# Optimization experiments

Measured on AMD Instinct MI355X. Metric: run time of the kernel, lower is better.

Reference implementation:

```python
import jax, jax.numpy as jnp
import numpy as np


def setup_inputs() -> dict:
    key = jax.random.key(0)
    k1, k2, k3, k4 = jax.random.split(key, 4)
    T, B, D_in, D_out = 512, 128, 512, 512
    X = jax.random.normal(k1, (T, B, D_in), dtype=jnp.float32)
    # torch nn.Linear default init: U(-1/sqrt(fan_in), 1/sqrt(fan_in))
    lim_in = 1.0 / np.sqrt(D_in)
    lim_h = 1.0 / np.sqrt(D_out)
    W_in = jax.random.uniform(k2, (D_out, D_in), jnp.float32, -lim_in, lim_in)
    W_h = jax.random.uniform(k3, (D_out, D_out), jnp.float32, -lim_h, lim_h)
    b_h = jax.random.uniform(k4, (D_out,), jnp.float32, -lim_h, lim_h)
    return {"X": X, "W_in": W_in, "W_h": W_h, "b_h": b_h}


def reference(X, W_in, W_h, b_h):
    # X: [T, B, D_in]. h_{t+1} = sigmoid(x_t @ W_in^T + h_t @ W_h^T + b_h)
    B = X.shape[1]
    D_out = W_h.shape[0]
    # Precompute all input projections in one big GEMM (same math).
    Xproj = jnp.einsum('tbi,oi->tbo', X, W_in)  # [T, B, D_out]
    h0 = jnp.zeros((B, D_out), dtype=X.dtype)

    def step(h, xp):
        h_new = jax.nn.sigmoid(xp + h @ W_h.T + b_h)
        return h_new, None

    h_last, _ = jax.lax.scan(step, h0, Xproj)
    return h_last
```

## Files before the change

### kernel.cpp

```cpp
#include <hip/hip_runtime.h>
#include <hip/hip_bf16.h>
#include <stdint.h>

typedef _Float16 f16;
typedef _Float16 f16x2 __attribute__((ext_vector_type(2)));
typedef _Float16 f16x4 __attribute__((ext_vector_type(4)));
typedef _Float16 f16x8 __attribute__((ext_vector_type(8)));
typedef float f32x4 __attribute__((ext_vector_type(4)));
typedef int   i32x4 __attribute__((ext_vector_type(4)));

#define T_STEPS 512
#define BATCH   128
#define DD      512
#define LOG2E   1.44269504088896f

#define XP_OFF  0
#define WF_OFF  (67108864)
#define WHQ_OFF (67108864 + 524288)
#define SC_OFF  (67108864 + 524288 + 262144)

__device__ __forceinline__ f16x2 pk(float a, float b) {
    return __builtin_bit_cast(f16x2, __builtin_amdgcn_cvt_pkrtz(a, b));
}

__device__ __forceinline__ float fast_exp2(float x) {
#if __has_builtin(__builtin_amdgcn_exp2f)
    return __builtin_amdgcn_exp2f(x);
#else
    return exp2f(x);
#endif
}

__device__ __forceinline__ float fast_rcp(float x) {
#if __has_builtin(__builtin_amdgcn_rcpf)
    return __builtin_amdgcn_rcpf(x);
#else
    return 1.0f / x;
#endif
}

__device__ __forceinline__ uint32_t pack_u8(float s, int pos, uint32_t old) {
#if __has_builtin(__builtin_amdgcn_cvt_pk_u8_f32)
    return __builtin_amdgcn_cvt_pk_u8_f32(s, pos, old);
#else
    return old | (((uint32_t)(int)s & 0xFF) << (8 * pos));
#endif
}

#define GLDS(g, l) __builtin_amdgcn_global_load_lds(                               \
        (const __attribute__((address_space(1))) void*)(g),                        \
        (__attribute__((address_space(3))) void*)(l), 16, 0, 0)

__global__ __launch_bounds__(256) void prep_kernel(
        const float* __restrict__ Win, f16* __restrict__ Wf) {
    int idx = blockIdx.x * 256 + threadIdx.x;
    if (idx < 262144) Wf[idx] = (f16)Win[idx];
}

__global__ __launch_bounds__(64) void quant_kernel(
        const float* __restrict__ Wh, char* __restrict__ Whq, float* __restrict__ scales) {
    const int o = blockIdx.x, t = threadIdx.x;
    const float* row = Wh + (size_t)o * 512;
    float v[8];
    float m = 0.f;
#pragma unroll
    for (int j = 0; j < 8; j++) { v[j] = row[t * 8 + j]; m = fmaxf(m, fabsf(v[j])); }
#pragma unroll
    for (int off = 32; off > 0; off >>= 1) m = fmaxf(m, __shfl_xor(m, off));
    if (t == 0) scales[o] = -LOG2E * m * (1.0f / (127.0f * 127.0f));
    const float inv = 127.0f / m;
    const int rt = o >> 4, rl = o & 15;
    const int k0 = t * 8;
    const int ks = k0 >> 6, qq = (k0 >> 4) & 3, j0 = k0 & 15;
    const int l = qq * 16 + rl;
    char* dst = Whq + ((size_t)((rt * 8 + ks) * 64 + l)) * 16 + j0;
#pragma unroll
    for (int j = 0; j < 8; j++) dst[j] = (char)rintf(v[j] * inv);
}

__global__ __launch_bounds__(512, 4) void gemm_kernel(
        const float* __restrict__ X, const f16* __restrict__ Wf,
        const float* __restrict__ bias, f16* __restrict__ Xp) {
    const int tid = threadIdx.x;
    const int l = tid & 63, w = tid >> 6;
    const int q = l >> 4, rl = l & 15;
    const int wm = w >> 2, wn = w & 3;
    const int blk = blockIdx.x;
    const int xcd = blk & 7, idx = blk >> 3;
    const int m_blk = (xcd * 64 + (idx >> 2)) * 128;
    const int n_blk = (idx & 3) * 128;

    __shared__ __align__(16) float As[2][128 * 32];
    __shared__ __align__(16) f16   Bs[2][128 * 32];

    const float* aSrc[2];
#pragma unroll
    for (int c = 0; c < 2; c++)
        aSrc[c] = X + (size_t)(m_blk + w * 16 + c * 8 + (l >> 3)) * 512
                    + (((l & 7) ^ (l >> 3)) << 2);
    const f16* bSrc = Wf + (size_t)(n_blk + w * 16 + (l >> 2)) * 512
                         + (((l & 3) ^ ((l >> 3) & 3)) << 3);

    f32x4 acc[4][2] = {};
    const int swA0 = (((2 * q)     ^ (rl & 7)) << 2);
    const int swA1 = (((2 * q + 1) ^ (rl & 7)) << 2);
    const int swB  = ((q ^ ((rl >> 1) & 3)) << 3);

#pragma unroll
    for (int c = 0; c < 2; c++) GLDS(aSrc[c], &As[0][(w * 16 + c * 8) * 32]);
    GLDS(bSrc, &Bs[0][(w * 16) * 32]);

    for (int t = 0; t < 16; ++t) {
        const int cur = t & 1;
        __syncthreads();
        if (t < 15) {
            const int kf = (t + 1) * 32;
#pragma unroll
            for (int c = 0; c < 2; c++) GLDS(aSrc[c] + kf, &As[cur ^ 1][(w * 16 + c * 8) * 32]);
            GLDS(bSrc + kf, &Bs[cur ^ 1][(w * 16) * 32]);
        }
        f16x8 af4[4], bf4[2];
#pragma unroll
        for (int i = 0; i < 4; i++) {
            const int row = wm * 64 + i * 16 + rl;
            const float4 h0 = *(const float4*)&As[cur][row * 32 + swA0];
            const float4 h1 = *(const float4*)&As[cur][row * 32 + swA1];
            f16x2 p0 = pk(h0.x, h0.y), p1 = pk(h0.z, h0.w);
            f16x2 p2 = pk(h1.x, h1.y), p3 = pk(h1.z, h1.w);
            f16x8 tv;
            tv[0] = p0[0]; tv[1] = p0[1]; tv[2] = p1[0]; tv[3] = p1[1];
            tv[4] = p2[0]; tv[5] = p2[1]; tv[6] = p3[0]; tv[7] = p3[1];
            af4[i] = tv;
        }
#pragma unroll
        for (int j = 0; j < 2; j++) {
            const int row = wn * 32 + j * 16 + rl;
            bf4[j] = *(const f16x8*)&Bs[cur][row * 32 + swB];
        }
#pragma unroll
        for (int i = 0; i < 4; i++)
#pragma unroll
            for (int j = 0; j < 2; j++)
                acc[i][j] = __builtin_amdgcn_mfma_f32_16x16x32_f16(bf4[j], af4[i], acc[i][j], 0, 0, 0);
    }
#pragma unroll
    for (int j = 0; j < 2; j++) {
        const float4 b4 = *(const float4*)&bias[n_blk + wn * 32 + j * 16 + q * 4];
        const float bb[4] = {b4.x, b4.y, b4.z, b4.w};
#pragma unroll
        for (int i = 0; i < 4; i++) {
            const int m = m_blk + wm * 64 + i * 16 + rl;
            f16x4 v;
#pragma unroll
            for (int r = 0; r < 4; r++)
                v[r] = (f16)(-LOG2E * (acc[i][j][r] + bb[r]));
            *(f16x4*)(Xp + (size_t)m * 512 + n_blk + wn * 32 + j * 16 + q * 4) = v;
        }
    }
}

__global__ __launch_bounds__(1024) void rnn_kernel(
        const char* __restrict__ Whq, const float* __restrict__ scales,
        const f16* __restrict__ Xp, float* __restrict__ out) {
    const int wg = blockIdx.x;
    const int tid = threadIdx.x;
    const int l = tid & 63, w = tid >> 6;
    const int bl = l & 15;
    const int q = l >> 4;
    const int b = wg * 16 + bl;

    __shared__ __align__(16) uint32_t hT[2][2048];

    i32x4 af[2][8];
    {
        const i32x4* wp = (const i32x4*)Whq;
#pragma unroll
        for (int mt = 0; mt < 2; mt++)
#pragma unroll
            for (int ks = 0; ks < 8; ks++)
                af[mt][ks] = wp[((w * 2 + mt) * 8 + ks) * 64 + l];
    }
    float sc[2][4];
#pragma unroll
    for (int mt = 0; mt < 2; mt++)
#pragma unroll
        for (int r = 0; r < 4; r++)
            sc[mt][r] = scales[w * 32 + mt * 16 + q * 4 + r];

    for (int i = tid; i < 2048; i += 1024) hT[0][i] = 0u;
    __syncthreads();

    const f16* xpb = Xp + (size_t)b * 512 + w * 32 + q * 4;
    f16x4 xn0 = *(const f16x4*)(xpb);
    f16x4 xn1 = *(const f16x4*)(xpb + 16);

    const float K127 = 1.0f / 127.0f;
    for (int t = 0; t < T_STEPS; t++) {
        f16x4 xc0 = xn0, xc1 = xn1;
        const size_t tn = (size_t)(t < T_STEPS - 1 ? t + 1 : t) * (BATCH * 512);
        xn0 = *(const f16x4*)(xpb + tn);
        xn1 = *(const f16x4*)(xpb + tn + 16);

        const int rb = t & 1;
        const uint32_t* hrow = &hT[rb][l * 4];
        uint32_t* hwr = &hT[1 - rb][w * 128 + bl * 4 + q];

        i32x4 bfr[8];
#pragma unroll
        for (int ks = 0; ks < 8; ks++)
            bfr[ks] = *(const i32x4*)(hrow + ks * 256);

        i32x4 acc0 = {}, acc1 = {};
        __builtin_amdgcn_s_setprio(1);
#pragma unroll
        for (int ks = 0; ks < 8; ks++)
            acc0 = __builtin_amdgcn_mfma_i32_16x16x64_i8(af[0][ks], bfr[ks], acc0, 0, 0, 0);

        uint32_t pk0 = 0;
#pragma unroll
        for (int r = 0; r < 4; r++) {
            float tt = fmaf((float)acc0[r], sc[0][r], (float)xc0[r]);
            float e  = fast_exp2(tt);
            float eq = fmaf(e, K127, K127);
            float sg = fast_rcp(eq) + 0.5f;
            pk0 = pack_u8(sg, r, pk0);
        }
        hwr[0] = pk0;

#pragma unroll
        for (int ks = 0; ks < 8; ks++)
            acc1 = __builtin_amdgcn_mfma_i32_16x16x64_i8(af[1][ks], bfr[ks], acc1, 0, 0, 0);
        __builtin_amdgcn_s_setprio(0);

        uint32_t pk1 = 0;
#pragma unroll
        for (int r = 0; r < 4; r++) {
            float tt = fmaf((float)acc1[r], sc[1][r], (float)xc1[r]);
            float e  = fast_exp2(tt);
            float eq = fmaf(e, K127, K127);
            float sg = fast_rcp(eq) + 0.5f;
            pk1 = pack_u8(sg, r, pk1);
        }
        hwr[64] = pk1;
        __syncthreads();
    }
#pragma unroll
    for (int mt = 0; mt < 2; mt++) {
        uint32_t pkq = hT[T_STEPS & 1][w * 128 + mt * 64 + bl * 4 + q];
        float4 o;
        o.x = (float)((pkq      ) & 0xFF) * K127;
        o.y = (float)((pkq >>  8) & 0xFF) * K127;
        o.z = (float)((pkq >> 16) & 0xFF) * K127;
        o.w = (float)((pkq >> 24) & 0xFF) * K127;
        *(float4*)(out + (size_t)b * 512 + w * 32 + mt * 16 + q * 4) = o;
    }
}

extern "C" void kernel_launch(void* const* d_in, const int* in_sizes, int n_in,
                              void* d_out, int out_size, void* d_ws, size_t ws_size,
                              hipStream_t stream) {
    const float* X   = (const float*)d_in[0];
    const float* Win = (const float*)d_in[1];
    const float* Wh  = (const float*)d_in[2];
    const float* bh  = (const float*)d_in[3];
    float* out = (float*)d_out;
    char* ws = (char*)d_ws;
    f16* Xp      = (f16*)(ws + XP_OFF);
    f16* Wf      = (f16*)(ws + WF_OFF);
    char* Whq    = (char*)(ws + WHQ_OFF);
    float* Sc    = (float*)(ws + SC_OFF);

    prep_kernel<<<1024, 256, 0, stream>>>(Win, Wf);
    quant_kernel<<<512, 64, 0, stream>>>(Wh, Whq, Sc);
    gemm_kernel<<<2048, 512, 0, stream>>>(X, Wf, bh, Xp);
    rnn_kernel<<<8, 1024, 0, stream>>>(Whq, Sc, Xp, out);
}
```

Measured before the change: 707.8 us.

## Halve RNN workgroup to 8 waves and retile input-projection GEMM to 64x128

The recurrent kernel now uses 8 waves per workgroup instead of 16. Each wave holds four 16-row output tiles of the int8 weight in registers and runs 32 MFMAs per step, which halves the number of waves meeting at each per-step barrier. The GEMM is retiled to 64x128 blocks with 256 threads and 4096 blocks, with each wave computing a 32x64 sub-tile. The intent is to cut per-timestep synchronisation cost in the serial recurrence, at the price of a longer MFMA chain per wave and doubled weight-register pressure.

```diff
diff --git a/kernel.cpp b/kernel.cpp
--- a/kernel.cpp
+++ b/kernel.cpp
@@ -78,19 +78,19 @@
     for (int j = 0; j < 8; j++) dst[j] = (char)rintf(v[j] * inv);
 }
 
-__global__ __launch_bounds__(512, 4) void gemm_kernel(
+__global__ __launch_bounds__(256, 4) void gemm_kernel(
         const float* __restrict__ X, const f16* __restrict__ Wf,
         const float* __restrict__ bias, f16* __restrict__ Xp) {
     const int tid = threadIdx.x;
     const int l = tid & 63, w = tid >> 6;
     const int q = l >> 4, rl = l & 15;
-    const int wm = w >> 2, wn = w & 3;
+    const int wm = w >> 1, wn = w & 1;
     const int blk = blockIdx.x;
     const int xcd = blk & 7, idx = blk >> 3;
-    const int m_blk = (xcd * 64 + (idx >> 2)) * 128;
+    const int m_blk = (xcd * 128 + (idx >> 2)) * 64;
     const int n_blk = (idx & 3) * 128;
 
-    __shared__ __align__(16) float As[2][128 * 32];
+    __shared__ __align__(16) float As[2][64 * 32];
     __shared__ __align__(16) f16   Bs[2][128 * 32];
 
     const float* aSrc[2];
@@ -98,17 +98,21 @@
     for (int c = 0; c < 2; c++)
         aSrc[c] = X + (size_t)(m_blk + w * 16 + c * 8 + (l >> 3)) * 512
                     + (((l & 7) ^ (l >> 3)) << 2);
-    const f16* bSrc = Wf + (size_t)(n_blk + w * 16 + (l >> 2)) * 512
-                         + (((l & 3) ^ ((l >> 3) & 3)) << 3);
-
-    f32x4 acc[4][2] = {};
+    const f16* bSrc[2];
+#pragma unroll
+    for (int c = 0; c < 2; c++)
+        bSrc[c] = Wf + (size_t)(n_blk + c * 64 + w * 16 + (l >> 2)) * 512
+                     + (((l & 3) ^ ((l >> 3) & 3)) << 3);
+
+    f32x4 acc[2][4] = {};
     const int swA0 = (((2 * q)     ^ (rl & 7)) << 2);
     const int swA1 = (((2 * q + 1) ^ (rl & 7)) << 2);
     const int swB  = ((q ^ ((rl >> 1) & 3)) << 3);
 
 #pragma unroll
     for (int c = 0; c < 2; c++) GLDS(aSrc[c], &As[0][(w * 16 + c * 8) * 32]);
-    GLDS(bSrc, &Bs[0][(w * 16) * 32]);
+#pragma unroll
+    for (int c = 0; c < 2; c++) GLDS(bSrc[c], &Bs[0][(c * 64 + w * 16) * 32]);
 
     for (int t = 0; t < 16; ++t) {
         const int cur = t & 1;
@@ -117,12 +121,13 @@
             const int kf = (t + 1) * 32;
 #pragma unroll
             for (int c = 0; c < 2; c++) GLDS(aSrc[c] + kf, &As[cur ^ 1][(w * 16 + c * 8) * 32]);
-            GLDS(bSrc + kf, &Bs[cur ^ 1][(w * 16) * 32]);
-        }
-        f16x8 af4[4], bf4[2];
-#pragma unroll
-        for (int i = 0; i < 4; i++) {
-            const int row = wm * 64 + i * 16 + rl;
+#pragma unroll
+            for (int c = 0; c < 2; c++) GLDS(bSrc[c] + kf, &Bs[cur ^ 1][(c * 64 + w * 16) * 32]);
+        }
+        f16x8 af4[2], bf4[4];
+#pragma unroll
+        for (int i = 0; i < 2; i++) {
+            const int row = wm * 32 + i * 16 + rl;
             const float4 h0 = *(const float4*)&As[cur][row * 32 + swA0];
             const float4 h1 = *(const float4*)&As[cur][row * 32 + swA1];
             f16x2 p0 = pk(h0.x, h0.y), p1 = pk(h0.z, h0.w);
@@ -133,33 +138,33 @@
             af4[i] = tv;
         }
 #pragma unroll
-        for (int j = 0; j < 2; j++) {
-            const int row = wn * 32 + j * 16 + rl;
+        for (int j = 0; j < 4; j++) {
+            const int row = wn * 64 + j * 16 + rl;
             bf4[j] = *(const f16x8*)&Bs[cur][row * 32 + swB];
         }
 #pragma unroll
-        for (int i = 0; i < 4; i++)
-#pragma unroll
-            for (int j = 0; j < 2; j++)
+        for (int i = 0; i < 2; i++)
+#pragma unroll
+            for (int j = 0; j < 4; j++)
                 acc[i][j] = __builtin_amdgcn_mfma_f32_16x16x32_f16(bf4[j], af4[i], acc[i][j], 0, 0, 0);
     }
 #pragma unroll
-    for (int j = 0; j < 2; j++) {
-        const float4 b4 = *(const float4*)&bias[n_blk + wn * 32 + j * 16 + q * 4];
+    for (int j = 0; j < 4; j++) {
+        const float4 b4 = *(const float4*)&bias[n_blk + wn * 64 + j * 16 + q * 4];
         const float bb[4] = {b4.x, b4.y, b4.z, b4.w};
 #pragma unroll
-        for (int i = 0; i < 4; i++) {
-            const int m = m_blk + wm * 64 + i * 16 + rl;
+        for (int i = 0; i < 2; i++) {
+            const int m = m_blk + wm * 32 + i * 16 + rl;
             f16x4 v;
 #pragma unroll
             for (int r = 0; r < 4; r++)
                 v[r] = (f16)(-LOG2E * (acc[i][j][r] + bb[r]));
-            *(f16x4*)(Xp + (size_t)m * 512 + n_blk + wn * 32 + j * 16 + q * 4) = v;
-        }
-    }
-}
-
-__global__ __launch_bounds__(1024) void rnn_kernel(
+            *(f16x4*)(Xp + (size_t)m * 512 + n_blk + wn * 64 + j * 16 + q * 4) = v;
+        }
+    }
+}
+
+__global__ __launch_bounds__(512, 2) void rnn_kernel(
         const char* __restrict__ Whq, const float* __restrict__ scales,
         const f16* __restrict__ Xp, float* __restrict__ out) {
     const int wg = blockIdx.x;
@@ -171,88 +176,78 @@
 
     __shared__ __align__(16) uint32_t hT[2][2048];
 
-    i32x4 af[2][8];
+    i32x4 af[4][8];
     {
         const i32x4* wp = (const i32x4*)Whq;
 #pragma unroll
-        for (int mt = 0; mt < 2; mt++)
+        for (int mt = 0; mt < 4; mt++)
 #pragma unroll
             for (int ks = 0; ks < 8; ks++)
-                af[mt][ks] = wp[((w * 2 + mt) * 8 + ks) * 64 + l];
-    }
-    float sc[2][4];
-#pragma unroll
-    for (int mt = 0; mt < 2; mt++)
+                af[mt][ks] = wp[((w * 4 + mt) * 8 + ks) * 64 + l];
+    }
+    float sc[4][4];
+#pragma unroll
+    for (int mt = 0; mt < 4; mt++)
 #pragma unroll
         for (int r = 0; r < 4; r++)
-            sc[mt][r] = scales[w * 32 + mt * 16 + q * 4 + r];
-
-    for (int i = tid; i < 2048; i += 1024) hT[0][i] = 0u;
+            sc[mt][r] = scales[w * 64 + mt * 16 + q * 4 + r];
+
+    for (int i = tid; i < 2048; i += 512) hT[0][i] = 0u;
     __syncthreads();
 
-    const f16* xpb = Xp + (size_t)b * 512 + w * 32 + q * 4;
-    f16x4 xn0 = *(const f16x4*)(xpb);
-    f16x4 xn1 = *(const f16x4*)(xpb + 16);
+    const f16* xpb = Xp + (size_t)b * 512 + w * 64 + q * 4;
+    f16x4 xn[4];
+#pragma unroll
+    for (int mt = 0; mt < 4; mt++) xn[mt] = *(const f16x4*)(xpb + mt * 16);
 
     const float K127 = 1.0f / 127.0f;
     for (int t = 0; t < T_STEPS; t++) {
-        f16x4 xc0 = xn0, xc1 = xn1;
+        f16x4 xc[4];
+#pragma unroll
+        for (int mt = 0; mt < 4; mt++) xc[mt] = xn[mt];
         const size_t tn = (size_t)(t < T_STEPS - 1 ? t + 1 : t) * (BATCH * 512);
-        xn0 = *(const f16x4*)(xpb + tn);
-        xn1 = *(const f16x4*)(xpb + tn + 16);
+#pragma unroll
+        for (int mt = 0; mt < 4; mt++) xn[mt] = *(const f16x4*)(xpb + tn + mt * 16);
 
         const int rb = t & 1;
         const uint32_t* hrow = &hT[rb][l * 4];
-        uint32_t* hwr = &hT[1 - rb][w * 128 + bl * 4 + q];
+        uint32_t* hwr = &hT[1 - rb][w * 256 + bl * 4 + q];
 
         i32x4 bfr[8];
 #pragma unroll
         for (int ks = 0; ks < 8; ks++)
             bfr[ks] = *(const i32x4*)(hrow + ks * 256);
 
-        i32x4 acc0 = {}, acc1 = {};
-        __builtin_amdgcn_s_setprio(1);
-#pragma unroll
-        for (int ks = 0; ks < 8; ks++)
-            acc0 = __builtin_amdgcn_mfma_i32_16x16x64_i8(af[0][ks], bfr[ks], acc0, 0, 0, 0);
-
-        uint32_t pk0 = 0;
-#pragma unroll
-        for (int r = 0; r < 4; r++) {
-            float tt = fmaf((float)acc0[r], sc[0][r], (float)xc0[r]);
-            float e  = fast_exp2(tt);
-            float eq = fmaf(e, K127, K127);
-            float sg = fast_rcp(eq) + 0.5f;
-            pk0 = pack_u8(sg, r, pk0);
-        }
-        hwr[0] = pk0;
-
-#pragma unroll
-        for (int ks = 0; ks < 8; ks++)
-            acc1 = __builtin_amdgcn_mfma_i32_16x16x64_i8(af[1][ks], bfr[ks], acc1, 0, 0, 0);
-        __builtin_amdgcn_s_setprio(0);
-
-        uint32_t pk1 = 0;
-#pragma unroll
-        for (int r = 0; r < 4; r++) {
-            float tt = fmaf((float)acc1[r], sc[1][r], (float)xc1[r]);
-            float e  = fast_exp2(tt);
-            float eq = fmaf(e, K127, K127);
-            float sg = fast_rcp(eq) + 0.5f;
-            pk1 = pack_u8(sg, r, pk1);
-        }
-        hwr[64] = pk1;
+#pragma unroll
+        for (int mt = 0; mt < 4; mt++) {
+            i32x4 acc = {};
+            __builtin_amdgcn_s_setprio(1);
+#pragma unroll
+            for (int ks = 0; ks < 8; ks++)
+                acc = __builtin_amdgcn_mfma_i32_16x16x64_i8(af[mt][ks], bfr[ks], acc, 0, 0, 0);
+            __builtin_amdgcn_s_setprio(0);
+            uint32_t pkq = 0;
+#pragma unroll
+            for (int r = 0; r < 4; r++) {
+                float tt = fmaf((float)acc[r], sc[mt][r], (float)xc[mt][r]);
+                float e  = fast_exp2(tt);
+                float eq = fmaf(e, K127, K127);
+                float sg = fast_rcp(eq) + 0.5f;
+                pkq = pack_u8(sg, r, pkq);
+            }
+            hwr[mt * 64] = pkq;
+        }
         __syncthreads();
     }
 #pragma unroll
-    for (int mt = 0; mt < 2; mt++) {
-        uint32_t pkq = hT[T_STEPS & 1][w * 128 + mt * 64 + bl * 4 + q];
+    for (int mt = 0; mt < 4; mt++) {
+        uint32_t pkq = hT[T_STEPS & 1][w * 256 + (mt * 16 + bl) * 4 + q];
         float4 o;
         o.x = (float)((pkq      ) & 0xFF) * K127;
         o.y = (float)((pkq >>  8) & 0xFF) * K127;
         o.z = (float)((pkq >> 16) & 0xFF) * K127;
         o.w = (float)((pkq >> 24) & 0xFF) * K127;
-        *(float4*)(out + (size_t)b * 512 + w * 32 + mt * 16 + q * 4) = o;
+        *(float4*)(out + (size_t)b * 512 + w * 64 + mt * 16 + q * 4) = o;
     }
 }
 
@@ -272,6 +267,6 @@
 
     prep_kernel<<<1024, 256, 0, stream>>>(Win, Wf);
     quant_kernel<<<512, 64, 0, stream>>>(Wh, Whq, Sc);
-    gemm_kernel<<<2048, 512, 0, stream>>>(X, Wf, bh, Xp);
-    rnn_kernel<<<8, 1024, 0, stream>>>(Whq, Sc, Xp, out);
-}
+    gemm_kernel<<<4096, 256, 0, stream>>>(X, Wf, bh, Xp);
+    rnn_kernel<<<8, 512, 0, stream>>>(Whq, Sc, Xp, out);
+}
```

After: 870.3 us. 23.0% more time.
